# Optimization experiments

Measured on AMD Instinct MI355X. Metric: run time of the kernel, lower is better.

The kernel has to match this reference:

```python
import jax, jax.numpy as jnp
import numpy as np

B, S, D = 8, 1024, 768
H = 12
DH = D // H  # 64


def setup_inputs() -> dict:
    key = jax.random.key(0)
    ks = jax.random.split(key, 9)
    s = 0.02
    return {
        "x": jax.random.normal(ks[0], (B, S, D), dtype=jnp.float32),
        # per-head QKV projections stacked over heads: [H, D, DH]
        "Wq": jax.random.normal(ks[1], (H, D, DH), dtype=jnp.float32) * s,
        "bq": jax.random.normal(ks[2], (H, DH), dtype=jnp.float32) * s,
        "Wk": jax.random.normal(ks[3], (H, D, DH), dtype=jnp.float32) * s,
        "bk": jax.random.normal(ks[4], (H, DH), dtype=jnp.float32) * s,
        "Wv": jax.random.normal(ks[5], (H, D, DH), dtype=jnp.float32) * s,
        "bv": jax.random.normal(ks[6], (H, DH), dtype=jnp.float32) * s,
        # output projection: [D, D] (applied as x @ Wo + bo)
        "Wo": jax.random.normal(ks[7], (D, D), dtype=jnp.float32) * s,
        "bo": jax.random.normal(ks[8], (D,), dtype=jnp.float32) * s,
    }


def reference(x, Wq, bq, Wk, bk, Wv, bv, Wo, bo):
    # Per-head linear projections, vectorized over heads -> [B, H, S, DH]
    q = jnp.einsum("bsd,hde->bhse", x, Wq) + bq[None, :, None, :]
    k = jnp.einsum("bsd,hde->bhse", x, Wk) + bk[None, :, None, :]
    v = jnp.einsum("bsd,hde->bhse", x, Wv) + bv[None, :, None, :]
    scale = 1.0 / jnp.sqrt(jnp.asarray(DH, dtype=q.dtype))
    scores = jnp.einsum("bhse,bhte->bhst", q, k) * scale  # [B,H,S,S]
    probs = jax.nn.softmax(scores, axis=-1)  # dropout p=0 (eval)
    out = jnp.einsum("bhst,bhte->bhse", probs, v)  # [B,H,S,DH]
    # concat heads (head order matches ModuleList order) -> [B,S,D]
    out = out.transpose(0, 2, 1, 3).reshape(B, S, D)
    return out @ Wo + bo
```

## Files before the change

### kernel.cpp

```cpp
#include <hip/hip_runtime.h>
#include <math.h>

#define BB 8
#define SS 1024
#define DD 768
#define HH 12
#define DHH 64
#define BSS (BB*SS)
#define NQKV 2304
#define NT 24

typedef _Float16 half8 __attribute__((ext_vector_type(8)));
typedef _Float16 half4 __attribute__((ext_vector_type(4)));
typedef float    f32x4 __attribute__((ext_vector_type(4)));

__device__ __forceinline__ void glds16(const _Float16* g, _Float16* l)
{
    __builtin_amdgcn_global_load_lds(
        (const __attribute__((address_space(1))) uint32_t*)(g),
        (__attribute__((address_space(3))) uint32_t*)(l),
        16, 0, 0);
}

__global__ __launch_bounds__(256)
void prep(const float* __restrict__ x, _Float16* __restrict__ xh,
          const float* __restrict__ Wq, const float* __restrict__ Wk,
          const float* __restrict__ Wv, const float* __restrict__ Wo,
          _Float16* __restrict__ Wt, _Float16* __restrict__ Wot)
{
    const int blk = blockIdx.x;
    const int tid = threadIdx.x;

    if (blk < 3072) {
        int i = blk * 256 + tid;
        const float4* xp = (const float4*)x + (size_t)i * 2;
        float4 u = xp[0], v = xp[1];
        half8 h = { (_Float16)u.x, (_Float16)u.y, (_Float16)u.z, (_Float16)u.w,
                    (_Float16)v.x, (_Float16)v.y, (_Float16)v.z, (_Float16)v.w };
        ((half8*)xh)[i] = h;
        return;
    }

    __shared__ float T[64][65];
    const int t  = blk - 3072;
    const int z  = t / 144;
    const int r_ = t - z * 144;
    const int d0 = (r_ / 12) * 64;
    const int n_outer = r_ % 12;

    const float* src;
    _Float16* dst;
    int base_mul, row_stride;
    if (z < 3) {
        src = (z == 0) ? Wq : (z == 1) ? Wk : Wv;
        dst = Wt + (size_t)z * DD * DD;
        base_mul = DD * DHH; row_stride = DHH;
    } else {
        src = Wo; dst = Wot;
        base_mul = 64; row_stride = DD;
    }

    const size_t base = (size_t)n_outer * base_mul;
    {
        int dl = tid >> 2, c0 = (tid & 3) * 16;
        const float* p = src + base + (size_t)(d0 + dl) * row_stride + c0;
#pragma unroll
        for (int m = 0; m < 4; ++m) {
            float4 f = *(const float4*)(p + m * 4);
            T[dl][c0 + m*4 + 0] = f.x;
            T[dl][c0 + m*4 + 1] = f.y;
            T[dl][c0 + m*4 + 2] = f.z;
            T[dl][c0 + m*4 + 3] = f.w;
        }
    }
    __syncthreads();
    {
        int e = tid >> 2, c = tid & 3;
        half8 lo, hi;
#pragma unroll
        for (int i = 0; i < 8; ++i) {
            lo[i] = (_Float16)T[c*16 + i][e];
            hi[i] = (_Float16)T[c*16 + 8 + i][e];
        }
        _Float16* q = dst + ((size_t)n_outer * 64 + e) * DD + d0 + c * 16;
        *(half8*)q = lo;
        *(half8*)(q + 8) = hi;
    }
}

__global__ __launch_bounds__(512, 2)
void gemm_qkv_256(const _Float16* __restrict__ Xh, const _Float16* __restrict__ Wt,
                  const float* __restrict__ bq, const float* __restrict__ bk,
                  const float* __restrict__ bv,
                  _Float16* __restrict__ qo, _Float16* __restrict__ ko,
                  _Float16* __restrict__ vto)
{
    __shared__ _Float16 Ab[4][256][32];
    __shared__ _Float16 Bb[4][256][32];

    const int bid = blockIdx.x;
    const int c = bid & 7;
    const int g = bid >> 3;
    const int m0 = (c * 4 + g / 9) * 256;
    const int n0 = (g % 9) * 256;

    const int tid  = threadIdx.x;
    const int wave = tid >> 6;
    const int lane = tid & 63;
    const int l16  = tid & 15;
    const int quad = (tid >> 4) & 3;
    const int wy = wave >> 2;
    const int wx = wave & 3;

    const int scol = ((lane & 3) ^ ((lane >> 3) & 3)) * 8;
    const _Float16* ap0 = Xh + (size_t)(m0 + wave * 32 + (lane >> 2)) * DD + scol;
    const _Float16* bp0 = Wt + (size_t)(n0 + wave * 32 + (lane >> 2)) * DD + scol;

    const int fcol = (quad ^ ((l16 >> 1) & 3)) * 8;

    f32x4 acc[8][4];
#pragma unroll
    for (int i = 0; i < 8; ++i)
#pragma unroll
        for (int j = 0; j < 4; ++j) acc[i][j] = (f32x4){0.f, 0.f, 0.f, 0.f};

#pragma unroll
    for (int t = 0; t < 3; ++t) {
        glds16(ap0 + t * 32,           &Ab[t][wave * 32][0]);
        glds16(ap0 + t * 32 + 16 * DD, &Ab[t][wave * 32 + 16][0]);
        glds16(bp0 + t * 32,           &Bb[t][wave * 32][0]);
        glds16(bp0 + t * 32 + 16 * DD, &Bb[t][wave * 32 + 16][0]);
    }
    asm volatile("s_waitcnt vmcnt(8)\n\ts_barrier" ::: "memory");

#pragma unroll 4
    for (int kt = 0; kt < NT; ++kt) {
        const int bf = kt & 3;

        half8 a[8], bA[2];
#pragma unroll
        for (int i = 0; i < 8; ++i)
            a[i] = *(const half8*)&Ab[bf][wy * 128 + i * 16 + l16][fcol];
#pragma unroll
        for (int j = 0; j < 2; ++j)
            bA[j] = *(const half8*)&Bb[bf][wx * 64 + j * 16 + l16][fcol];
        if (kt + 3 < NT) {
            const int nf = (kt + 3) & 3;
            glds16(ap0 + (kt + 3) * 32,           &Ab[nf][wave * 32][0]);
            glds16(ap0 + (kt + 3) * 32 + 16 * DD, &Ab[nf][wave * 32 + 16][0]);
        }
        __builtin_amdgcn_s_setprio(1);
#pragma unroll
        for (int i = 0; i < 8; ++i) {
            acc[i][0] = __builtin_amdgcn_mfma_f32_16x16x32_f16(a[i], bA[0], acc[i][0], 0, 0, 0);
            acc[i][1] = __builtin_amdgcn_mfma_f32_16x16x32_f16(a[i], bA[1], acc[i][1], 0, 0, 0);
        }
        __builtin_amdgcn_s_setprio(0);

        half8 bB[2];
#pragma unroll
        for (int j = 0; j < 2; ++j)
            bB[j] = *(const half8*)&Bb[bf][wx * 64 + (2 + j) * 16 + l16][fcol];
        if (kt + 3 < NT) {
            const int nf = (kt + 3) & 3;
            glds16(bp0 + (kt + 3) * 32,           &Bb[nf][wave * 32][0]);
            glds16(bp0 + (kt + 3) * 32 + 16 * DD, &Bb[nf][wave * 32 + 16][0]);
        }
        __builtin_amdgcn_s_setprio(1);
#pragma unroll
        for (int i = 0; i < 8; ++i) {
            acc[i][2] = __builtin_amdgcn_mfma_f32_16x16x32_f16(a[i], bB[0], acc[i][2], 0, 0, 0);
            acc[i][3] = __builtin_amdgcn_mfma_f32_16x16x32_f16(a[i], bB[1], acc[i][3], 0, 0, 0);
        }
        __builtin_amdgcn_s_setprio(0);

        if (kt < NT - 3)
            asm volatile("s_waitcnt vmcnt(8)\n\ts_barrier" ::: "memory");
        else if (kt == NT - 3)
            asm volatile("s_waitcnt vmcnt(4)\n\ts_barrier" ::: "memory");
        else if (kt == NT - 2)
            asm volatile("s_waitcnt vmcnt(0)\n\ts_barrier" ::: "memory");
    }

    const int wsel  = n0 / 768;
    const int ncol0 = n0 - wsel * 768 + wx * 64;

    if (wsel == 0) {
#pragma unroll
        for (int i = 0; i < 8; ++i) {
#pragma unroll
            for (int r = 0; r < 4; ++r) {
                int row = m0 + wy * 128 + i * 16 + quad * 4 + r;
                int b_ = row >> 10;
                int s  = row & (SS - 1);
#pragma unroll
                for (int j = 0; j < 4; ++j) {
                    int nl = ncol0 + j * 16 + l16;
                    int h = nl >> 6, e = nl & 63;
                    float val = (acc[i][j][r] + bq[nl]) * 0.125f;
                    qo[((size_t)(b_ * HH + h) * SS + s) * DHH + e] = (_Float16)val;
                }
            }
        }
    } else if (wsel == 1) {
#pragma unroll
        for (int i = 0; i < 8; ++i) {
#pragma unroll
            for (int r = 0; r < 4; ++r) {
                int row = m0 + wy * 128 + i * 16 + quad * 4 + r;
                int b_ = row >> 10;
                int s  = row & (SS - 1);
#pragma unroll
                for (int j = 0; j < 4; ++j) {
                    int nl = ncol0 + j * 16 + l16;
                    int h = nl >> 6, e = nl & 63;
                    float val = acc[i][j][r] + bk[nl];
                    ko[((size_t)(b_ * HH + h) * SS + s) * DHH + e] = (_Float16)val;
                }
            }
        }
    } else {
#pragma unroll
        for (int i = 0; i < 8; ++i) {
#pragma unroll
            for (int r = 0; r < 4; ++r) {
                int row = m0 + wy * 128 + i * 16 + quad * 4 + r;
                int b_ = row >> 10;
                int s  = row & (SS - 1);
#pragma unroll
                for (int j = 0; j < 4; ++j) {
                    int nl = ncol0 + j * 16 + l16;
                    int h = nl >> 6, e = nl & 63;
                    float val = acc[i][j][r] + bv[nl];
                    vto[((size_t)(b_ * HH + h) * DHH + e) * SS + s] = (_Float16)val;
                }
            }
        }
    }
}

__global__ __launch_bounds__(256)
void gemm_out_f16(const _Float16* __restrict__ Ah, const _Float16* __restrict__ Bt,
                  const float* __restrict__ bias, float* __restrict__ out)
{
    __shared__ _Float16 Ash[2][128][32];
    __shared__ _Float16 Bsh[2][64][32];

    const int m0 = blockIdx.x * 128;
    const int n0 = blockIdx.y * 64;
    const int tid  = threadIdx.x;
    const int wave = tid >> 6;
    const int lane = tid & 63;
    const int l16  = tid & 15;
    const int quad = (tid >> 4) & 3;
    const int wy = wave >> 1;
    const int wx = wave & 1;

    const int scol = ((lane & 3) ^ ((lane >> 3) & 3)) * 8;
    const int fcol = (quad ^ ((l16 >> 1) & 3)) * 8;

    const _Float16* ap = Ah + (size_t)(m0 + 32 * wave + (lane >> 2)) * DD + scol;
    const _Float16* bp = Bt + (size_t)(n0 + 16 * wave + (lane >> 2)) * DD + scol;

    f32x4 acc[4][2];
#pragma unroll
    for (int i = 0; i < 4; ++i)
#pragma unroll
        for (int j = 0; j < 2; ++j) acc[i][j] = (f32x4){0.f, 0.f, 0.f, 0.f};

    glds16(ap, &Ash[0][32 * wave][0]);
    glds16(ap + 16 * DD, &Ash[0][32 * wave + 16][0]);
    glds16(bp, &Bsh[0][16 * wave][0]);

    int cur = 0;
    for (int k0 = 0; k0 < DD; k0 += 32) {
        __syncthreads();
        if (k0 + 32 < DD) {
            glds16(ap + k0 + 32, &Ash[cur ^ 1][32 * wave][0]);
            glds16(ap + k0 + 32 + 16 * DD, &Ash[cur ^ 1][32 * wave + 16][0]);
            glds16(bp + k0 + 32, &Bsh[cur ^ 1][16 * wave][0]);
        }

        half8 a[4], bf[2];
#pragma unroll
        for (int i = 0; i < 4; ++i)
            a[i] = *(const half8*)&Ash[cur][wy * 64 + i * 16 + l16][fcol];
#pragma unroll
        for (int j = 0; j < 2; ++j)
            bf[j] = *(const half8*)&Bsh[cur][wx * 32 + j * 16 + l16][fcol];
#pragma unroll
        for (int i = 0; i < 4; ++i)
#pragma unroll
            for (int j = 0; j < 2; ++j)
                acc[i][j] = __builtin_amdgcn_mfma_f32_16x16x32_f16(a[i], bf[j], acc[i][j], 0, 0, 0);
        cur ^= 1;
    }

#pragma unroll
    for (int i = 0; i < 4; ++i) {
#pragma unroll
        for (int r = 0; r < 4; ++r) {
            int row = m0 + wy * 64 + i * 16 + quad * 4 + r;
#pragma unroll
            for (int j = 0; j < 2; ++j) {
                int col = n0 + wx * 32 + j * 16 + l16;
                out[(size_t)row * DD + col] = acc[i][j][r] + bias[col];
            }
        }
    }
}

__global__ __launch_bounds__(512)
void attn_f16(const _Float16* __restrict__ qh, const _Float16* __restrict__ kh,
              const _Float16* __restrict__ vt, _Float16* __restrict__ ctxh)
{
    const int bh  = blockIdx.x;
    const int q0  = blockIdx.y * 128;
    const int tid = threadIdx.x;
    const int wave = tid >> 6;
    const int lane = tid & 63;
    const int l16  = tid & 15;
    const int quad = (tid >> 4) & 3;

    __shared__ _Float16 Ks[2][2][64][32];
    __shared__ _Float16 Vt[2][2][64][32];
    __shared__ _Float16 Pt[8][16][72];

    const int scol = ((lane & 3) ^ ((lane >> 3) & 3)) * 8;
    const int fcol = (quad ^ ((l16 >> 1) & 3)) * 8;

    const _Float16* qrow = qh + ((size_t)bh * SS + q0 + wave * 16 + l16) * DHH;
    const half8 qlo = *(const half8*)(qrow + quad * 8);
    const half8 qhi = *(const half8*)(qrow + 32 + quad * 8);

    const int sw = wave & 3;
    const _Float16* kp = kh + ((size_t)bh * SS + 16 * sw + (lane >> 2)) * DHH + scol;
    const _Float16* vp = vt + ((size_t)bh * DHH + 16 * sw + (lane >> 2)) * SS + scol;

    f32x4 o[4];
    float lacc = 0.f;
#pragma unroll
    for (int j = 0; j < 4; ++j) o[j] = (f32x4){0.f, 0.f, 0.f, 0.f};

    if (wave < 4) {
        glds16(kp,      &Ks[0][0][16 * sw][0]);
        glds16(kp + 32, &Ks[0][1][16 * sw][0]);
    } else {
        glds16(vp,      &Vt[0][0][16 * sw][0]);
        glds16(vp + 32, &Vt[0][1][16 * sw][0]);
    }

    int cur = 0;
    for (int kt = 0; kt < SS; kt += 64) {
        __syncthreads();
        if (kt + 64 < SS) {
            if (wave < 4) {
                glds16(kp + (size_t)(kt + 64) * DHH,      &Ks[cur ^ 1][0][16 * sw][0]);
                glds16(kp + (size_t)(kt + 64) * DHH + 32, &Ks[cur ^ 1][1][16 * sw][0]);
            } else {
                glds16(vp + kt + 64,      &Vt[cur ^ 1][0][16 * sw][0]);
                glds16(vp + kt + 64 + 32, &Vt[cur ^ 1][1][16 * sw][0]);
            }
        }

#pragma unroll
        for (int f = 0; f < 4; ++f) {
            half8 klo = *(const half8*)&Ks[cur][0][f * 16 + l16][fcol];
            half8 khi = *(const half8*)&Ks[cur][1][f * 16 + l16][fcol];
            f32x4 z = (f32x4){0.f, 0.f, 0.f, 0.f};
            z = __builtin_amdgcn_mfma_f32_16x16x32_f16(klo, qlo, z, 0, 0, 0);
            z = __builtin_amdgcn_mfma_f32_16x16x32_f16(khi, qhi, z, 0, 0, 0);
            half4 pk;
#pragma unroll
            for (int r = 0; r < 4; ++r) {
                float p = __expf(z[r]);
                lacc += p;
                pk[r] = (_Float16)p;
            }
            *(half4*)&Pt[wave][l16][f * 16 + quad * 4] = pk;
        }

        half8 pl = *(const half8*)&Pt[wave][l16][quad * 8];
        half8 ph = *(const half8*)&Pt[wave][l16][32 + quad * 8];

#pragma unroll
        for (int j = 0; j < 4; ++j) {
            half8 vlo = *(const half8*)&Vt[cur][0][j * 16 + l16][fcol];
            half8 vhi = *(const half8*)&Vt[cur][1][j * 16 + l16][fcol];
            o[j] = __builtin_amdgcn_mfma_f32_16x16x32_f16(pl, vlo, o[j], 0, 0, 0);
            o[j] = __builtin_amdgcn_mfma_f32_16x16x32_f16(ph, vhi, o[j], 0, 0, 0);
        }
        cur ^= 1;
    }

    float lr = lacc;
    lr += __shfl_xor(lr, 16);
    lr += __shfl_xor(lr, 32);

    const int b_ = bh / HH;
    const int h_ = bh % HH;
#pragma unroll
    for (int r = 0; r < 4; ++r) {
        float invl = 1.f / __shfl(lr, quad * 4 + r, 16);
        int s_ = q0 + wave * 16 + quad * 4 + r;
        _Float16* orow = ctxh + ((size_t)(b_ * SS + s_)) * DD + h_ * DHH;
#pragma unroll
        for (int j = 0; j < 4; ++j)
            orow[j * 16 + l16] = (_Float16)(o[j][r] * invl);
    }
}

extern "C" void kernel_launch(void* const* d_in, const int* in_sizes, int n_in,
                              void* d_out, int out_size, void* d_ws, size_t ws_size,
                              hipStream_t stream)
{
    const float* x  = (const float*)d_in[0];
    const float* Wq = (const float*)d_in[1];
    const float* bq = (const float*)d_in[2];
    const float* Wk = (const float*)d_in[3];
    const float* bk = (const float*)d_in[4];
    const float* Wv = (const float*)d_in[5];
    const float* bv = (const float*)d_in[6];
    const float* Wo = (const float*)d_in[7];
    const float* bo = (const float*)d_in[8];
    float* out = (float*)d_out;

    const size_t xe = (size_t)BSS * DD;
    const size_t we = (size_t)DD * DD;
    _Float16* Xh   = (_Float16*)d_ws;
    _Float16* Wt   = Xh  + xe;
    _Float16* Wot  = Wt  + (size_t)3 * we;
    _Float16* qhb  = Wot + we;
    _Float16* khb  = qhb + xe;
    _Float16* vtb  = khb + xe;
    _Float16* ctxh = vtb + xe;

    prep<<<3072 + 576, 256, 0, stream>>>(x, Xh, Wq, Wk, Wv, Wo, Wt, Wot);

    gemm_qkv_256<<<(BSS / 256) * (NQKV / 256), 512, 0, stream>>>(
        Xh, Wt, bq, bk, bv, qhb, khb, vtb);

    dim3 ag(BB * HH, SS / 128);
    attn_f16<<<ag, 512, 0, stream>>>(qhb, khb, vtb, ctxh);

    dim3 gg(BSS / 128, DD / 64);
    gemm_out_f16<<<gg, 256, 0, stream>>>(ctxh, Wot, bo, out);
}
```

Baseline: 201.4 us.

## Restructure QKV GEMM into 8-phase double-buffered K64 pipeline and reorder attention loads

The QKV projection GEMM moves from a 4-deep K=32 ring buffer to a double-buffered K=64 tile split into four phases. Each phase interleaves LDS reads, global-to-LDS staging and MFMA groups, with explicit barriers and an 8-way XOR swizzle. Bias and head/index values are hoisted out of the epilogue loops. In the attention kernel, all QK MFMAs and V loads are issued before the exp/softmax work to expose more latency hiding. The cost is more barriers per K step and higher register pressure.

```diff
diff --git a/kernel.cpp b/kernel.cpp
--- a/kernel.cpp
+++ b/kernel.cpp
@@ -9,6 +9,7 @@
 #define BSS (BB*SS)
 #define NQKV 2304
 #define NT 24
+#define NT64 12
 
 typedef _Float16 half8 __attribute__((ext_vector_type(8)));
 typedef _Float16 half4 __attribute__((ext_vector_type(4)));
@@ -21,6 +22,9 @@
         (__attribute__((address_space(3))) uint32_t*)(l),
         16, 0, 0);
 }
+
+#define WAITV(N) asm volatile("s_waitcnt vmcnt(" #N ")" ::: "memory")
+#define MF(a, b, c) __builtin_amdgcn_mfma_f32_16x16x32_f16(a, b, c, 0, 0, 0)
 
 __global__ __launch_bounds__(256)
 void prep(const float* __restrict__ x, _Float16* __restrict__ xh,
@@ -89,34 +93,50 @@
 }
 
 __global__ __launch_bounds__(512, 2)
-void gemm_qkv_256(const _Float16* __restrict__ Xh, const _Float16* __restrict__ Wt,
+void gemm_qkv_8ph(const _Float16* __restrict__ Xh, const _Float16* __restrict__ Wt,
                   const float* __restrict__ bq, const float* __restrict__ bk,
                   const float* __restrict__ bv,
                   _Float16* __restrict__ qo, _Float16* __restrict__ ko,
                   _Float16* __restrict__ vto)
 {
-    __shared__ _Float16 Ab[4][256][32];
-    __shared__ _Float16 Bb[4][256][32];
+    __shared__ _Float16 Ab[2][2][128][64];
+    __shared__ _Float16 Bb[2][2][128][64];
 
     const int bid = blockIdx.x;
-    const int c = bid & 7;
-    const int g = bid >> 3;
-    const int m0 = (c * 4 + g / 9) * 256;
-    const int n0 = (g % 9) * 256;
+    const int c8  = bid & 7;
+    const int g   = bid >> 3;
+    const int m_t = c8 * 4 + g / 9;
+    const int n_t = g % 9;
+    const int m0 = m_t * 256;
+    const int n0 = n_t * 256;
 
     const int tid  = threadIdx.x;
     const int wave = tid >> 6;
     const int lane = tid & 63;
     const int l16  = tid & 15;
     const int quad = (tid >> 4) & 3;
+    const int l7   = l16 & 7;
     const int wy = wave >> 2;
     const int wx = wave & 3;
 
-    const int scol = ((lane & 3) ^ ((lane >> 3) & 3)) * 8;
-    const _Float16* ap0 = Xh + (size_t)(m0 + wave * 32 + (lane >> 2)) * DD + scol;
-    const _Float16* bp0 = Wt + (size_t)(n0 + wave * 32 + (lane >> 2)) * DD + scol;
-
-    const int fcol = (quad ^ ((l16 >> 1) & 3)) * 8;
+    const int scol = ((lane & 7) ^ ((lane >> 3) & 7)) * 8;
+
+    const _Float16* apS = Xh + (size_t)(m0 + wave * 32 + (lane >> 3)) * DD + scol;
+    const _Float16* bpS = Wt + (size_t)(n0 + wave * 32 + (lane >> 3)) * DD + scol;
+    const int sh = wave >> 2;
+    const int sr = (wave & 3) * 32;
+
+#define STAGE_A(nb, t1) do { _Pragma("unroll")                              \
+    for (int i_ = 0; i_ < 4; ++i_)                                          \
+        glds16(apS + (size_t)i_ * 8 * DD + (t1) * 64,                       \
+               &Ab[nb][sh][sr + i_ * 8][0]); } while (0)
+#define STAGE_B(nb, t1) do { _Pragma("unroll")                              \
+    for (int i_ = 0; i_ < 4; ++i_)                                          \
+        glds16(bpS + (size_t)i_ * 8 * DD + (t1) * 64,                       \
+               &Bb[nb][sh][sr + i_ * 8][0]); } while (0)
+
+#define RD_A(buf, m, ks) (*(const half8*)&Ab[buf][wy][(m)*16 + l16][((((ks)*4 + quad)) ^ l7) * 8])
+#define RD_B(buf, j, ks) (*(const half8*)&Bb[buf][wx >> 1][(wx & 1)*64 + (j)*16 + l16][((((ks)*4 + quad)) ^ l7) * 8])
 
     f32x4 acc[8][4];
 #pragma unroll
@@ -124,70 +144,72 @@
 #pragma unroll
         for (int j = 0; j < 4; ++j) acc[i][j] = (f32x4){0.f, 0.f, 0.f, 0.f};
 
-#pragma unroll
-    for (int t = 0; t < 3; ++t) {
-        glds16(ap0 + t * 32,           &Ab[t][wave * 32][0]);
-        glds16(ap0 + t * 32 + 16 * DD, &Ab[t][wave * 32 + 16][0]);
-        glds16(bp0 + t * 32,           &Bb[t][wave * 32][0]);
-        glds16(bp0 + t * 32 + 16 * DD, &Bb[t][wave * 32 + 16][0]);
-    }
-    asm volatile("s_waitcnt vmcnt(8)\n\ts_barrier" ::: "memory");
-
-#pragma unroll 4
-    for (int kt = 0; kt < NT; ++kt) {
-        const int bf = kt & 3;
-
-        half8 a[8], bA[2];
+#define PHASE(buf, M0, STG, GATE)                                           \
+    {                                                                       \
+        half8 a00 = RD_A(buf, (M0), 0),     a01 = RD_A(buf, (M0), 1);       \
+        half8 a10 = RD_A(buf, (M0) + 1, 0), a11 = RD_A(buf, (M0) + 1, 1);   \
+        STG;                                                                \
+        __builtin_amdgcn_s_barrier();                                       \
+        asm volatile("s_waitcnt lgkmcnt(0)" ::: "memory");                  \
+        __builtin_amdgcn_sched_barrier(0);                                  \
+        __builtin_amdgcn_s_setprio(1);                                      \
+        _Pragma("unroll")                                                   \
+        for (int j = 0; j < 4; ++j) {                                       \
+            acc[(M0)][j]     = MF(a00, bf[j][0], acc[(M0)][j]);             \
+            acc[(M0)][j]     = MF(a01, bf[j][1], acc[(M0)][j]);             \
+            acc[(M0) + 1][j] = MF(a10, bf[j][0], acc[(M0) + 1][j]);         \
+            acc[(M0) + 1][j] = MF(a11, bf[j][1], acc[(M0) + 1][j]);         \
+        }                                                                   \
+        __builtin_amdgcn_s_setprio(0);                                      \
+        GATE;                                                               \
+        __builtin_amdgcn_s_barrier();                                       \
+    }
+
+    STAGE_A(0, 0); STAGE_B(0, 0);
+    WAITV(0);
+    __builtin_amdgcn_s_barrier();
+
+#pragma unroll 2
+    for (int t = 0; t < NT64; ++t) {
+        const int buf = t & 1;
+        const int nb  = buf ^ 1;
+        const bool stg = (t + 1 < NT64);
+
+        half8 bf[4][2];
+#pragma unroll
+        for (int j = 0; j < 4; ++j) {
+            bf[j][0] = RD_B(buf, j, 0);
+            bf[j][1] = RD_B(buf, j, 1);
+        }
+
+        PHASE(buf, 0, if (stg) STAGE_A(nb, t + 1), );
+        PHASE(buf, 2, if (stg) STAGE_B(nb, t + 1), );
+        PHASE(buf, 4, , );
+        PHASE(buf, 6, , if (stg) WAITV(0));
+    }
+
+#undef PHASE
+#undef RD_A
+#undef RD_B
+#undef STAGE_A
+#undef STAGE_B
+
+    const int wsel = n0 / 768;
+    const int nb_ = n0 - wsel * 768 + wx * 64;
+    const float* bp_ = (wsel == 0) ? bq : (wsel == 1) ? bk : bv;
+
+    float bvv[4]; int hh4[4], ee4[4];
+#pragma unroll
+    for (int j = 0; j < 4; ++j) {
+        int nl = nb_ + j * 16 + l16;
+        bvv[j] = bp_[nl];
+        hh4[j] = nl >> 6;
+        ee4[j] = nl & 63;
+    }
+
+    if (wsel == 0) {
 #pragma unroll
         for (int i = 0; i < 8; ++i)
-            a[i] = *(const half8*)&Ab[bf][wy * 128 + i * 16 + l16][fcol];
-#pragma unroll
-        for (int j = 0; j < 2; ++j)
-            bA[j] = *(const half8*)&Bb[bf][wx * 64 + j * 16 + l16][fcol];
-        if (kt + 3 < NT) {
-            const int nf = (kt + 3) & 3;
-            glds16(ap0 + (kt + 3) * 32,           &Ab[nf][wave * 32][0]);
-            glds16(ap0 + (kt + 3) * 32 + 16 * DD, &Ab[nf][wave * 32 + 16][0]);
-        }
-        __builtin_amdgcn_s_setprio(1);
-#pragma unroll
-        for (int i = 0; i < 8; ++i) {
-            acc[i][0] = __builtin_amdgcn_mfma_f32_16x16x32_f16(a[i], bA[0], acc[i][0], 0, 0, 0);
-            acc[i][1] = __builtin_amdgcn_mfma_f32_16x16x32_f16(a[i], bA[1], acc[i][1], 0, 0, 0);
-        }
-        __builtin_amdgcn_s_setprio(0);
-
-        half8 bB[2];
-#pragma unroll
-        for (int j = 0; j < 2; ++j)
-            bB[j] = *(const half8*)&Bb[bf][wx * 64 + (2 + j) * 16 + l16][fcol];
-        if (kt + 3 < NT) {
-            const int nf = (kt + 3) & 3;
-            glds16(bp0 + (kt + 3) * 32,           &Bb[nf][wave * 32][0]);
-            glds16(bp0 + (kt + 3) * 32 + 16 * DD, &Bb[nf][wave * 32 + 16][0]);
-        }
-        __builtin_amdgcn_s_setprio(1);
-#pragma unroll
-        for (int i = 0; i < 8; ++i) {
-            acc[i][2] = __builtin_amdgcn_mfma_f32_16x16x32_f16(a[i], bB[0], acc[i][2], 0, 0, 0);
-            acc[i][3] = __builtin_amdgcn_mfma_f32_16x16x32_f16(a[i], bB[1], acc[i][3], 0, 0, 0);
-        }
-        __builtin_amdgcn_s_setprio(0);
-
-        if (kt < NT - 3)
-            asm volatile("s_waitcnt vmcnt(8)\n\ts_barrier" ::: "memory");
-        else if (kt == NT - 3)
-            asm volatile("s_waitcnt vmcnt(4)\n\ts_barrier" ::: "memory");
-        else if (kt == NT - 2)
-            asm volatile("s_waitcnt vmcnt(0)\n\ts_barrier" ::: "memory");
-    }
-
-    const int wsel  = n0 / 768;
-    const int ncol0 = n0 - wsel * 768 + wx * 64;
-
-    if (wsel == 0) {
-#pragma unroll
-        for (int i = 0; i < 8; ++i) {
 #pragma unroll
             for (int r = 0; r < 4; ++r) {
                 int row = m0 + wy * 128 + i * 16 + quad * 4 + r;
@@ -195,16 +217,13 @@
                 int s  = row & (SS - 1);
 #pragma unroll
                 for (int j = 0; j < 4; ++j) {
-                    int nl = ncol0 + j * 16 + l16;
-                    int h = nl >> 6, e = nl & 63;
-                    float val = (acc[i][j][r] + bq[nl]) * 0.125f;
-                    qo[((size_t)(b_ * HH + h) * SS + s) * DHH + e] = (_Float16)val;
+                    float val = (acc[i][j][r] + bvv[j]) * 0.125f;
+                    qo[((size_t)(b_ * HH + hh4[j]) * SS + s) * DHH + ee4[j]] = (_Float16)val;
                 }
             }
-        }
     } else if (wsel == 1) {
 #pragma unroll
-        for (int i = 0; i < 8; ++i) {
+        for (int i = 0; i < 8; ++i)
 #pragma unroll
             for (int r = 0; r < 4; ++r) {
                 int row = m0 + wy * 128 + i * 16 + quad * 4 + r;
@@ -212,16 +231,13 @@
                 int s  = row & (SS - 1);
 #pragma unroll
                 for (int j = 0; j < 4; ++j) {
-                    int nl = ncol0 + j * 16 + l16;
-                    int h = nl >> 6, e = nl & 63;
-                    float val = acc[i][j][r] + bk[nl];
-                    ko[((size_t)(b_ * HH + h) * SS + s) * DHH + e] = (_Float16)val;
+                    float val = acc[i][j][r] + bvv[j];
+                    ko[((size_t)(b_ * HH + hh4[j]) * SS + s) * DHH + ee4[j]] = (_Float16)val;
                 }
             }
-        }
     } else {
 #pragma unroll
-        for (int i = 0; i < 8; ++i) {
+        for (int i = 0; i < 8; ++i)
 #pragma unroll
             for (int r = 0; r < 4; ++r) {
                 int row = m0 + wy * 128 + i * 16 + quad * 4 + r;
@@ -229,13 +245,10 @@
                 int s  = row & (SS - 1);
 #pragma unroll
                 for (int j = 0; j < 4; ++j) {
-                    int nl = ncol0 + j * 16 + l16;
-                    int h = nl >> 6, e = nl & 63;
-                    float val = acc[i][j][r] + bv[nl];
-                    vto[((size_t)(b_ * HH + h) * DHH + e) * SS + s] = (_Float16)val;
+                    float val = acc[i][j][r] + bvv[j];
+                    vto[((size_t)(b_ * HH + hh4[j]) * DHH + ee4[j]) * SS + s] = (_Float16)val;
                 }
             }
-        }
     }
 }
 
@@ -292,7 +305,7 @@
         for (int i = 0; i < 4; ++i)
 #pragma unroll
             for (int j = 0; j < 2; ++j)
-                acc[i][j] = __builtin_amdgcn_mfma_f32_16x16x32_f16(a[i], bf[j], acc[i][j], 0, 0, 0);
+                acc[i][j] = MF(a[i], bf[j], acc[i][j]);
         cur ^= 1;
     }
 
@@ -363,17 +376,29 @@
             }
         }
 
+        f32x4 z[4];
 #pragma unroll
         for (int f = 0; f < 4; ++f) {
             half8 klo = *(const half8*)&Ks[cur][0][f * 16 + l16][fcol];
             half8 khi = *(const half8*)&Ks[cur][1][f * 16 + l16][fcol];
-            f32x4 z = (f32x4){0.f, 0.f, 0.f, 0.f};
-            z = __builtin_amdgcn_mfma_f32_16x16x32_f16(klo, qlo, z, 0, 0, 0);
-            z = __builtin_amdgcn_mfma_f32_16x16x32_f16(khi, qhi, z, 0, 0, 0);
+            z[f] = (f32x4){0.f, 0.f, 0.f, 0.f};
+            z[f] = MF(klo, qlo, z[f]);
+            z[f] = MF(khi, qhi, z[f]);
+        }
+
+        half8 vv0[4], vv1[4];
+#pragma unroll
+        for (int j = 0; j < 4; ++j) {
+            vv0[j] = *(const half8*)&Vt[cur][0][j * 16 + l16][fcol];
+            vv1[j] = *(const half8*)&Vt[cur][1][j * 16 + l16][fcol];
+        }
+
+#pragma unroll
+        for (int f = 0; f < 4; ++f) {
             half4 pk;
 #pragma unroll
             for (int r = 0; r < 4; ++r) {
-                float p = __expf(z[r]);
+                float p = __expf(z[f][r]);
                 lacc += p;
                 pk[r] = (_Float16)p;
             }
@@ -385,10 +410,8 @@
 
 #pragma unroll
         for (int j = 0; j < 4; ++j) {
-            half8 vlo = *(const half8*)&Vt[cur][0][j * 16 + l16][fcol];
-            half8 vhi = *(const half8*)&Vt[cur][1][j * 16 + l16][fcol];
-            o[j] = __builtin_amdgcn_mfma_f32_16x16x32_f16(pl, vlo, o[j], 0, 0, 0);
-            o[j] = __builtin_amdgcn_mfma_f32_16x16x32_f16(ph, vhi, o[j], 0, 0, 0);
+            o[j] = MF(pl, vv0[j], o[j]);
+            o[j] = MF(ph, vv1[j], o[j]);
         }
         cur ^= 1;
     }
@@ -437,7 +460,7 @@
 
     prep<<<3072 + 576, 256, 0, stream>>>(x, Xh, Wq, Wk, Wv, Wo, Wt, Wot);
 
-    gemm_qkv_256<<<(BSS / 256) * (NQKV / 256), 512, 0, stream>>>(
+    gemm_qkv_8ph<<<(BSS / 256) * (NQKV / 256), 512, 0, stream>>>(
         Xh, Wt, bq, bk, bv, qhb, khb, vtb);
 
     dim3 ag(BB * HH, SS / 128);
```

After: 211.1 us. +4.8%, slower.

## Process two query tiles per wave in attention to reuse K/V fragments

Applied to the files above, without the earlier changes.

The attention kernel drops from 8 waves with 16 query rows each to 4 waves with 32 query rows each. Every K and V fragment read from LDS now feeds twice as many MFMAs, and all four waves load both K and V tiles. This cuts LDS read traffic and barrier participants per block. In exchange each wave uses more registers, and there are fewer waves per block to hide latency.

```diff
diff --git a/kernel.cpp b/kernel.cpp
--- a/kernel.cpp
+++ b/kernel.cpp
@@ -21,6 +21,8 @@
         (__attribute__((address_space(3))) uint32_t*)(l),
         16, 0, 0);
 }
+
+#define MF(a, b, c) __builtin_amdgcn_mfma_f32_16x16x32_f16(a, b, c, 0, 0, 0)
 
 __global__ __launch_bounds__(256)
 void prep(const float* __restrict__ x, _Float16* __restrict__ xh,
@@ -152,8 +154,8 @@
         __builtin_amdgcn_s_setprio(1);
 #pragma unroll
         for (int i = 0; i < 8; ++i) {
-            acc[i][0] = __builtin_amdgcn_mfma_f32_16x16x32_f16(a[i], bA[0], acc[i][0], 0, 0, 0);
-            acc[i][1] = __builtin_amdgcn_mfma_f32_16x16x32_f16(a[i], bA[1], acc[i][1], 0, 0, 0);
+            acc[i][0] = MF(a[i], bA[0], acc[i][0]);
+            acc[i][1] = MF(a[i], bA[1], acc[i][1]);
         }
         __builtin_amdgcn_s_setprio(0);
 
@@ -169,8 +171,8 @@
         __builtin_amdgcn_s_setprio(1);
 #pragma unroll
         for (int i = 0; i < 8; ++i) {
-            acc[i][2] = __builtin_amdgcn_mfma_f32_16x16x32_f16(a[i], bB[0], acc[i][2], 0, 0, 0);
-            acc[i][3] = __builtin_amdgcn_mfma_f32_16x16x32_f16(a[i], bB[1], acc[i][3], 0, 0, 0);
+            acc[i][2] = MF(a[i], bB[0], acc[i][2]);
+            acc[i][3] = MF(a[i], bB[1], acc[i][3]);
         }
         __builtin_amdgcn_s_setprio(0);
 
@@ -292,7 +294,7 @@
         for (int i = 0; i < 4; ++i)
 #pragma unroll
             for (int j = 0; j < 2; ++j)
-                acc[i][j] = __builtin_amdgcn_mfma_f32_16x16x32_f16(a[i], bf[j], acc[i][j], 0, 0, 0);
+                acc[i][j] = MF(a[i], bf[j], acc[i][j]);
         cur ^= 1;
     }
 
@@ -310,7 +312,7 @@
     }
 }
 
-__global__ __launch_bounds__(512)
+__global__ __launch_bounds__(256)
 void attn_f16(const _Float16* __restrict__ qh, const _Float16* __restrict__ kh,
               const _Float16* __restrict__ vt, _Float16* __restrict__ ctxh)
 {
@@ -323,90 +325,112 @@
     const int quad = (tid >> 4) & 3;
 
     __shared__ _Float16 Ks[2][2][64][32];
-    __shared__ _Float16 Vt[2][2][64][32];
-    __shared__ _Float16 Pt[8][16][72];
+    __shared__ _Float16 Vs[2][2][64][32];
+    __shared__ _Float16 Pt[4][32][72];
 
     const int scol = ((lane & 3) ^ ((lane >> 3) & 3)) * 8;
     const int fcol = (quad ^ ((l16 >> 1) & 3)) * 8;
 
-    const _Float16* qrow = qh + ((size_t)bh * SS + q0 + wave * 16 + l16) * DHH;
-    const half8 qlo = *(const half8*)(qrow + quad * 8);
-    const half8 qhi = *(const half8*)(qrow + 32 + quad * 8);
-
-    const int sw = wave & 3;
-    const _Float16* kp = kh + ((size_t)bh * SS + 16 * sw + (lane >> 2)) * DHH + scol;
-    const _Float16* vp = vt + ((size_t)bh * DHH + 16 * sw + (lane >> 2)) * SS + scol;
-
-    f32x4 o[4];
-    float lacc = 0.f;
-#pragma unroll
-    for (int j = 0; j < 4; ++j) o[j] = (f32x4){0.f, 0.f, 0.f, 0.f};
-
-    if (wave < 4) {
-        glds16(kp,      &Ks[0][0][16 * sw][0]);
-        glds16(kp + 32, &Ks[0][1][16 * sw][0]);
-    } else {
-        glds16(vp,      &Vt[0][0][16 * sw][0]);
-        glds16(vp + 32, &Vt[0][1][16 * sw][0]);
-    }
+    const _Float16* qrow0 = qh + ((size_t)bh * SS + q0 + wave * 32 + l16) * DHH;
+    const half8 qlo0 = *(const half8*)(qrow0 + quad * 8);
+    const half8 qhi0 = *(const half8*)(qrow0 + 32 + quad * 8);
+    const half8 qlo1 = *(const half8*)(qrow0 + 16 * DHH + quad * 8);
+    const half8 qhi1 = *(const half8*)(qrow0 + 16 * DHH + 32 + quad * 8);
+
+    const _Float16* kp = kh + ((size_t)bh * SS + 16 * wave + (lane >> 2)) * DHH + scol;
+    const _Float16* vp = vt + ((size_t)bh * DHH + 16 * wave + (lane >> 2)) * SS + scol;
+
+    f32x4 o0[4], o1[4];
+    float lacc0 = 0.f, lacc1 = 0.f;
+#pragma unroll
+    for (int j = 0; j < 4; ++j) {
+        o0[j] = (f32x4){0.f, 0.f, 0.f, 0.f};
+        o1[j] = (f32x4){0.f, 0.f, 0.f, 0.f};
+    }
+
+    glds16(kp,      &Ks[0][0][16 * wave][0]);
+    glds16(kp + 32, &Ks[0][1][16 * wave][0]);
+    glds16(vp,      &Vs[0][0][16 * wave][0]);
+    glds16(vp + 32, &Vs[0][1][16 * wave][0]);
 
     int cur = 0;
     for (int kt = 0; kt < SS; kt += 64) {
         __syncthreads();
         if (kt + 64 < SS) {
-            if (wave < 4) {
-                glds16(kp + (size_t)(kt + 64) * DHH,      &Ks[cur ^ 1][0][16 * sw][0]);
-                glds16(kp + (size_t)(kt + 64) * DHH + 32, &Ks[cur ^ 1][1][16 * sw][0]);
-            } else {
-                glds16(vp + kt + 64,      &Vt[cur ^ 1][0][16 * sw][0]);
-                glds16(vp + kt + 64 + 32, &Vt[cur ^ 1][1][16 * sw][0]);
-            }
-        }
-
+            glds16(kp + (size_t)(kt + 64) * DHH,      &Ks[cur ^ 1][0][16 * wave][0]);
+            glds16(kp + (size_t)(kt + 64) * DHH + 32, &Ks[cur ^ 1][1][16 * wave][0]);
+            glds16(vp + kt + 64,      &Vs[cur ^ 1][0][16 * wave][0]);
+            glds16(vp + kt + 64 + 32, &Vs[cur ^ 1][1][16 * wave][0]);
+        }
+
+        f32x4 z0[4], z1[4];
 #pragma unroll
         for (int f = 0; f < 4; ++f) {
             half8 klo = *(const half8*)&Ks[cur][0][f * 16 + l16][fcol];
             half8 khi = *(const half8*)&Ks[cur][1][f * 16 + l16][fcol];
-            f32x4 z = (f32x4){0.f, 0.f, 0.f, 0.f};
-            z = __builtin_amdgcn_mfma_f32_16x16x32_f16(klo, qlo, z, 0, 0, 0);
-            z = __builtin_amdgcn_mfma_f32_16x16x32_f16(khi, qhi, z, 0, 0, 0);
-            half4 pk;
+            z0[f] = (f32x4){0.f, 0.f, 0.f, 0.f};
+            z0[f] = MF(klo, qlo0, z0[f]);
+            z0[f] = MF(khi, qhi0, z0[f]);
+            z1[f] = (f32x4){0.f, 0.f, 0.f, 0.f};
+            z1[f] = MF(klo, qlo1, z1[f]);
+            z1[f] = MF(khi, qhi1, z1[f]);
+        }
+
+        half8 vv0[4], vv1[4];
+#pragma unroll
+        for (int j = 0; j < 4; ++j) {
+            vv0[j] = *(const half8*)&Vs[cur][0][j * 16 + l16][fcol];
+            vv1[j] = *(const half8*)&Vs[cur][1][j * 16 + l16][fcol];
+        }
+
+#pragma unroll
+        for (int f = 0; f < 4; ++f) {
+            half4 pk0, pk1;
 #pragma unroll
             for (int r = 0; r < 4; ++r) {
-                float p = __expf(z[r]);
-                lacc += p;
-                pk[r] = (_Float16)p;
+                float p0 = __expf(z0[f][r]); lacc0 += p0; pk0[r] = (_Float16)p0;
+                float p1 = __expf(z1[f][r]); lacc1 += p1; pk1[r] = (_Float16)p1;
             }
-            *(half4*)&Pt[wave][l16][f * 16 + quad * 4] = pk;
-        }
-
-        half8 pl = *(const half8*)&Pt[wave][l16][quad * 8];
-        half8 ph = *(const half8*)&Pt[wave][l16][32 + quad * 8];
+            *(half4*)&Pt[wave][l16][f * 16 + quad * 4]      = pk0;
+            *(half4*)&Pt[wave][16 + l16][f * 16 + quad * 4] = pk1;
+        }
+
+        half8 pl0 = *(const half8*)&Pt[wave][l16][quad * 8];
+        half8 ph0 = *(const half8*)&Pt[wave][l16][32 + quad * 8];
+        half8 pl1 = *(const half8*)&Pt[wave][16 + l16][quad * 8];
+        half8 ph1 = *(const half8*)&Pt[wave][16 + l16][32 + quad * 8];
 
 #pragma unroll
         for (int j = 0; j < 4; ++j) {
-            half8 vlo = *(const half8*)&Vt[cur][0][j * 16 + l16][fcol];
-            half8 vhi = *(const half8*)&Vt[cur][1][j * 16 + l16][fcol];
-            o[j] = __builtin_amdgcn_mfma_f32_16x16x32_f16(pl, vlo, o[j], 0, 0, 0);
-            o[j] = __builtin_amdgcn_mfma_f32_16x16x32_f16(ph, vhi, o[j], 0, 0, 0);
+            o0[j] = MF(pl0, vv0[j], o0[j]);
+            o0[j] = MF(ph0, vv1[j], o0[j]);
+            o1[j] = MF(pl1, vv0[j], o1[j]);
+            o1[j] = MF(ph1, vv1[j], o1[j]);
         }
         cur ^= 1;
     }
 
-    float lr = lacc;
-    lr += __shfl_xor(lr, 16);
-    lr += __shfl_xor(lr, 32);
+    float lr0 = lacc0;
+    lr0 += __shfl_xor(lr0, 16);
+    lr0 += __shfl_xor(lr0, 32);
+    float lr1 = lacc1;
+    lr1 += __shfl_xor(lr1, 16);
+    lr1 += __shfl_xor(lr1, 32);
 
     const int b_ = bh / HH;
     const int h_ = bh % HH;
 #pragma unroll
     for (int r = 0; r < 4; ++r) {
-        float invl = 1.f / __shfl(lr, quad * 4 + r, 16);
-        int s_ = q0 + wave * 16 + quad * 4 + r;
-        _Float16* orow = ctxh + ((size_t)(b_ * SS + s_)) * DD + h_ * DHH;
-#pragma unroll
-        for (int j = 0; j < 4; ++j)
-            orow[j * 16 + l16] = (_Float16)(o[j][r] * invl);
+        float inv0 = 1.f / __shfl(lr0, quad * 4 + r, 16);
+        float inv1 = 1.f / __shfl(lr1, quad * 4 + r, 16);
+        int s0_ = q0 + wave * 32 + quad * 4 + r;
+        _Float16* orow0 = ctxh + ((size_t)(b_ * SS + s0_)) * DD + h_ * DHH;
+        _Float16* orow1 = ctxh + ((size_t)(b_ * SS + s0_ + 16)) * DD + h_ * DHH;
+#pragma unroll
+        for (int j = 0; j < 4; ++j) {
+            orow0[j * 16 + l16] = (_Float16)(o0[j][r] * inv0);
+            orow1[j * 16 + l16] = (_Float16)(o1[j][r] * inv1);
+        }
     }
 }
 
@@ -441,7 +465,7 @@
         Xh, Wt, bq, bk, bv, qhb, khb, vtb);
 
     dim3 ag(BB * HH, SS / 128);
-    attn_f16<<<ag, 512, 0, stream>>>(qhb, khb, vtb, ctxh);
+    attn_f16<<<ag, 256, 0, stream>>>(qhb, khb, vtb, ctxh);
 
     dim3 gg(BSS / 128, DD / 64);
     gemm_out_f16<<<gg, 256, 0, stream>>>(ctxh, Wot, bo, out);
```

After: 205.1 us. No clear change (+1.8%).
